# Optimization experiments

Measured on AMD Instinct MI355X. Metric: run time of the kernel, lower is better.

Reference implementation:

```python
import jax, jax.numpy as jnp
import numpy as np

# ---- static config (mirrors GaussianLSS __init__) ----
ORF_H, ORF_W = 256, 704
FC, FH, FW = 128, 32, 88
D_ST, D_END, D_STEP = 4.0, 45.0, 1.0
OUT_C = 128
ERROR_TOL = 1.0
OPACITY_THR = 0.05
XB = (-50.0, 50.0, 1.0)
YB = (-50.0, 50.0, 1.0)
BEV_H = int(round((YB[1] - YB[0]) / YB[2]))
BEV_W = int(round((XB[1] - XB[0]) / XB[2]))
DS = np.arange(D_ST, D_END, D_STEP, dtype=np.float32)
D = DS.shape[0]  # 41
BN_EPS = 1e-3
CHUNK = 512      # gaussians composited per scan step (16896 = 33*512)
B, NCAM = 1, 6


def make_frustum():
    ds = jnp.broadcast_to(jnp.asarray(DS)[:, None, None], (D, FH, FW))
    xs = jnp.broadcast_to(jnp.linspace(0.0, ORF_W - 1.0, FW)[None, None, :], (D, FH, FW))
    ys = jnp.broadcast_to(jnp.linspace(0.0, ORF_H - 1.0, FH)[None, :, None], (D, FH, FW))
    return jnp.stack([xs, ys, ds], -1)  # [D,FH,FW,3]


def get_geometry(rots, trans, intrins, post_rots, post_trans):
    fr = make_frustum()
    pts = fr[None, None] - post_trans[:, :, None, None, None, :]
    pts = jnp.einsum('bnij,bndhwj->bndhwi', jnp.linalg.inv(post_rots), pts)
    pts = jnp.concatenate([pts[..., :2] * pts[..., 2:3], pts[..., 2:3]], -1)
    comb = jnp.einsum('bnij,bnjk->bnik', rots, jnp.linalg.inv(intrins))
    pts = jnp.einsum('bnij,bndhwj->bndhwi', comb, pts) + trans[:, :, None, None, None, :]
    return pts  # [B,N,D,FH,FW,3] ego-frame frustum points


def conv2d(x, w, b, pad):
    y = jax.lax.conv_general_dilated(x, w, (1, 1), [(pad, pad), (pad, pad)],
                                     dimension_numbers=('NCHW', 'OIHW', 'NCHW'))
    return y + b[None, :, None, None]


def bnorm(x, g, bt, m, v):
    s = (g / jnp.sqrt(v + BN_EPS))[None, :, None, None]
    return (x - m[None, :, None, None]) * s + bt[None, :, None, None]


def splat(means, cov6, colors, ops, valid_in):
    # Differentiable BEV gaussian rasterization (3DGS math, orthographic BEV camera,
    # all depths equal -> compositing in stable gaussian-index order).
    H, W = BEV_H, BEV_W
    sh, sw = H / 2.0, W / 2.0  # h/h_meters with FoV=2 (BEVCamera)
    my = -sh * means[:, 1] + H / 2.0  # pixel row (full_proj_transform row 0)
    mx = -sw * means[:, 0] + W / 2.0  # pixel col (row 1)
    a = sh * sh * cov6[:, 3] + 0.3    # 2D cov = J Sigma_xy J^T, +0.3 low-pass as in 3DGS
    c = sw * sw * cov6[:, 0] + 0.3
    b = sh * sw * cov6[:, 1]
    det = a * c - b * b
    valid = valid_in & (det > 0)
    inv_det = jnp.where(det > 0, 1.0 / det, 0.0)
    cA, cB, cC = c * inv_det, -b * inv_det, a * inv_det
    pi = jnp.repeat(jnp.arange(H, dtype=jnp.float32), W)  # [P] pixel rows
    pj = jnp.tile(jnp.arange(W, dtype=jnp.float32), H)    # [P] pixel cols
    G = means.shape[0]
    nchunk = G // CHUNK
    resh = lambda x: x.reshape((nchunk, CHUNK) + x.shape[1:])
    chunks = (resh(my), resh(mx), resh(cA), resh(cB), resh(cC),
              resh(ops), resh(valid), resh(colors))

    def body(carry, ch):
        logT, acc = carry
        my_c, mx_c, A, Bc, Cc, op_c, val_c, col_c = ch
        dI = pi[None, :] - my_c[:, None]                     # [Gc,P]
        dJ = pj[None, :] - mx_c[:, None]
        q = A[:, None] * dI * dI + 2.0 * Bc[:, None] * dI * dJ + Cc[:, None] * dJ * dJ
        alpha = jnp.minimum(0.99, op_c[:, None] * jnp.exp(-0.5 * q))
        alpha = jnp.where(val_c[:, None] & (q >= 0) & (alpha >= 1.0 / 255.0), alpha, 0.0)
        log1m = jnp.log1p(-alpha)
        cum = jnp.cumsum(log1m, axis=0)
        T = jnp.exp(logT[None, :] + cum - log1m)             # transmittance before each gaussian
        acc = acc + jnp.einsum('gp,gc->pc', alpha * T, col_c)
        return (logT + cum[-1], acc), None

    P = H * W
    init = (jnp.zeros((P,), jnp.float32), jnp.zeros((P, colors.shape[1]), jnp.float32))
    (_, acc), _ = jax.lax.scan(jax.checkpoint(body), init, chunks)
    return acc.reshape(H, W, -1).transpose(2, 0, 1)  # [C,H,W], bg is zeros


def _forward(cam2ego_rot, cam2ego_trans, cam_intrins, post_cam2ego_rot, post_cam2ego_trans,
             img_feats, conv1_w, conv1_b, bn1_g, bn1_b, bn1_m, bn1_v,
             conv2_w, conv2_b, bn2_g, bn2_b, bn2_m, bn2_v, conv3_w, conv3_b):
    geom = get_geometry(cam2ego_rot, cam2ego_trans, cam_intrins, post_cam2ego_rot, post_cam2ego_trans)
    b, n = img_feats.shape[:2]
    x = img_feats.reshape(b * n, FC, FH, FW)
    x = jax.nn.relu(bnorm(conv2d(x, conv1_w, conv1_b, 1), bn1_g, bn1_b, bn1_m, bn1_v))
    x = jax.nn.relu(bnorm(conv2d(x, conv2_w, conv2_b, 1), bn2_g, bn2_b, bn2_m, bn2_v))
    x = conv2d(x, conv3_w, conv3_b, 0)
    depth_prob = jax.nn.softmax(x[:, :D], axis=1).reshape(b, n, D, FH, FW)
    opac = jax.nn.sigmoid(x[:, D:D + 1]).reshape(b, n, FH, FW)
    feats = x[:, D + 1:].reshape(b, n, OUT_C, FH, FW)
    # per-pixel gaussian moments of the depth distribution (compute_gaussian)
    means = jnp.einsum('bndhw,bndhwi->bnhwi', depth_prob, geom)
    delta = means[:, :, None] - geom                                       # [B,N,D,FH,FW,3]
    cov = jnp.einsum('bndhw,bndhwi,bndhwj->bnhwij', depth_prob, delta, delta) * (ERROR_TOL ** 2 / 9.0)
    center = jnp.array([(XB[0] + XB[1]) / 2.0, (YB[0] + YB[1]) / 2.0, 0.0], jnp.float32)
    scale = jnp.array([2.0 / (XB[1] - XB[0]), 2.0 / (YB[1] - YB[0]), 1.0], jnp.float32)
    m_n = (means - center) * scale
    cov_n = cov * (scale[:, None] * scale[None, :])
    cov6 = jnp.stack([cov_n[..., 0, 0], cov_n[..., 0, 1], cov_n[..., 0, 2],
                      cov_n[..., 1, 1], cov_n[..., 1, 2], cov_n[..., 2, 2]], -1)
    g = n * FH * FW
    colors = feats.transpose(0, 1, 3, 4, 2).reshape(b, g, OUT_C)
    m_n = m_n.reshape(b, g, 3)
    cov6 = cov6.reshape(b, g, 6)
    ops = opac.reshape(b, g)
    mask = ops > OPACITY_THR  # opacity filtering == zero contribution, order preserved
    bev = jax.vmap(splat)(m_n, cov6, colors, ops, mask)                    # [B,C,H,W]
    num_gaussians = mask.astype(jnp.float32).sum(-1).mean()
    return bev, num_gaussians


def setup_inputs():
    key = jax.random.key(0)
    ks = jax.random.split(key, 8)
    # camera-to-ego rotations: cam->ego axis permutation composed with per-camera yaw
    yaw = np.linspace(0.0, 2.0 * np.pi, NCAM, endpoint=False).astype(np.float32)
    cz, sz = np.cos(yaw), np.sin(yaw)
    rotz = np.zeros((NCAM, 3, 3), np.float32)
    rotz[:, 0, 0] = cz; rotz[:, 0, 1] = -sz
    rotz[:, 1, 0] = sz; rotz[:, 1, 1] = cz
    rotz[:, 2, 2] = 1.0
    perm = np.array([[0.0, 0.0, 1.0], [-1.0, 0.0, 0.0], [0.0, -1.0, 0.0]], np.float32)
    rots = np.einsum('nij,jk->nik', rotz, perm)
    cam2ego_rot = jnp.asarray(np.broadcast_to(rots, (B, NCAM, 3, 3)).copy())
    cam2ego_trans = jax.random.normal(ks[0], (B, NCAM, 3), jnp.float32)
    K = np.array([[600.0, 0.0, ORF_W / 2.0], [0.0, 600.0, ORF_H / 2.0], [0.0, 0.0, 1.0]], np.float32)
    cam_intrins = jnp.asarray(np.broadcast_to(K, (B, NCAM, 3, 3)).copy())
    post_cam2ego_rot = jnp.broadcast_to(jnp.eye(3, dtype=jnp.float32), (B, NCAM, 3, 3)) + jnp.zeros((B, NCAM, 3, 3), jnp.float32)
    post_cam2ego_trans = jnp.zeros((B, NCAM, 3), jnp.float32)
    img_feats = jax.random.normal(ks[1], (B, NCAM, FC, FH, FW), jnp.float32)
    def conv_init(k, o, i, kh, kw):
        return jax.random.normal(k, (o, i, kh, kw), jnp.float32) * (1.0 / np.sqrt(i * kh * kw))
    return dict(cam2ego_rot=cam2ego_rot, cam2ego_trans=cam2ego_trans, cam_intrins=cam_intrins,
                post_cam2ego_rot=post_cam2ego_rot, post_cam2ego_trans=post_cam2ego_trans,
                img_feats=img_feats,
                conv1_w=conv_init(ks[2], FC, FC, 3, 3), conv1_b=jnp.zeros((FC,), jnp.float32),
                bn1_g=jnp.ones((FC,), jnp.float32), bn1_b=jnp.zeros((FC,), jnp.float32),
                bn1_m=jnp.zeros((FC,), jnp.float32), bn1_v=jnp.ones((FC,), jnp.float32),
                conv2_w=conv_init(ks[3], FC, FC, 3, 3), conv2_b=jnp.zeros((FC,), jnp.float32),
                bn2_g=jnp.ones((FC,), jnp.float32), bn2_b=jnp.zeros((FC,), jnp.float32),
                bn2_m=jnp.zeros((FC,), jnp.float32), bn2_v=jnp.ones((FC,), jnp.float32),
                conv3_w=conv_init(ks[4], OUT_C + D + 1, FC, 1, 1),
                conv3_b=jax.random.normal(ks[5], (OUT_C + D + 1,), jnp.float32) * 0.1)


def reference(cam2ego_rot, cam2ego_trans, cam_intrins, post_cam2ego_rot, post_cam2ego_trans,
              img_feats, conv1_w, conv1_b, bn1_g, bn1_b, bn1_m, bn1_v,
              conv2_w, conv2_b, bn2_g, bn2_b, bn2_m, bn2_v, conv3_w, conv3_b):
    return _forward(cam2ego_rot, cam2ego_trans, cam_intrins, post_cam2ego_rot, post_cam2ego_trans,
                    img_feats, conv1_w, conv1_b, bn1_g, bn1_b, bn1_m, bn1_v,
                    conv2_w, conv2_b, bn2_g, bn2_b, bn2_m, bn2_v, conv3_w, conv3_b)
```

## Files before the change

### kernel.cpp

```cpp
#include <hip/hip_runtime.h>

#define NCAM 6
#define FC   128
#define FH_  32
#define FW_  88
#define NPIX (FH_*FW_)
#define PH   34
#define PW   92
#define PPIX (PH*PW)
#define ND   41
#define X3D  42
#define OUTC 128
#define GTOT (NCAM*NPIX)
#define BEVH 100
#define BEVW 100
#define NPXB (BEVH*BEVW)
#define NTILE 25
#define NWORD 264
#define NMASKW (NTILE*NTILE*NWORD)
#define WCAP  70000
#define CSIZE 64
#define CBLK  2048

#define SZA     (NCAM*FC*PPIX)
#define WS_CAM  0
#define WS_A    256
#define WS_RB   (WS_A  + SZA)
#define WS_X3   (WS_RB + SZA)
#define WS_GS   (WS_X3 + NCAM*X3D*NPIX)
#define WS_WL   (WS_GS + GTOT*8)
#define WS_BASE (WS_WL + WCAP)

typedef __attribute__((ext_vector_type(8))) short bf16x8;
typedef __attribute__((ext_vector_type(4))) float f32x4;

__device__ inline unsigned short f2bf(float f) {
    unsigned u = __float_as_uint(f);
    u += 0x7fffu + ((u >> 16) & 1u);
    return (unsigned short)(u >> 16);
}

__device__ inline void inv3x3(const float* m, float* o) {
    float a=m[0],b=m[1],c=m[2],d=m[3],e=m[4],f=m[5],g=m[6],h=m[7],i=m[8];
    float A=e*i-f*h, B=c*h-b*i, C=b*f-c*e;
    float Dd=f*g-d*i, E=a*i-c*g, F=c*d-a*f;
    float Gg=d*h-e*g, H=b*g-a*h, I=a*e-b*d;
    float r = 1.0f/(a*A + b*Dd + c*Gg);
    o[0]=A*r; o[1]=B*r; o[2]=C*r; o[3]=Dd*r; o[4]=E*r; o[5]=F*r;
    o[6]=Gg*r; o[7]=H*r; o[8]=I*r;
}

__global__ __launch_bounds__(256) void pad_input_kernel(const float* __restrict__ src,
        float* __restrict__ dst, float* __restrict__ rb,
        float* __restrict__ outp, unsigned long long* __restrict__ masks) {
    int idx = blockIdx.x*256 + threadIdx.x;
    if (idx < NMASKW) masks[idx] = 0ull;
    if (idx <= NPXB*OUTC) outp[idx] = 0.0f;
    if (idx >= NCAM*FC*PPIX) return;
    int plane = idx / PPIX, pp = idx - plane*PPIX;
    int y = pp / PW, x = pp - y*PW;
    bool interior = (y >= 1 && y <= FH_ && x >= 1 && x <= FW_);
    float v = 0.0f;
    if (interior)
        v = src[(size_t)plane*NPIX + (y-1)*FW_ + (x-1)];
    dst[idx] = v;
    if (!interior) rb[idx] = 0.0f;
}

__global__ __launch_bounds__(128) void conv3x3_pf_kernel(
        const float* __restrict__ in, float* __restrict__ out, const float* __restrict__ w,
        const float* __restrict__ cb, const float* __restrict__ bg, const float* __restrict__ bb,
        const float* __restrict__ bm, const float* __restrict__ bv) {
    const int n   = blockIdx.x;
    const int co0 = blockIdx.y * 4;
    const int qid = blockIdx.z * 128 + threadIdx.x;
    if (qid >= 704) return;
    const int y = qid / 22, x0 = (qid - y*22) * 4;
    float scale[4], shift[4];
    #pragma unroll
    for (int c=0;c<4;c++) {
        float s = bg[co0+c] * rsqrtf(bv[co0+c] + 1e-3f);
        scale[c] = s;
        shift[c] = (cb[co0+c] - bm[co0+c]) * s + bb[co0+c];
    }
    float acc[4][4] = {};
    const float* ip = in + (size_t)n*FC*PPIX + y*PW + x0;
    const float* wb = w + (size_t)co0*FC*9;
    float4 p4[3]; float2 p2[3];
    #pragma unroll
    for (int r=0;r<3;r++) {
        p4[r] = *(const float4*)(ip + r*PW);
        p2[r] = *(const float2*)(ip + r*PW + 4);
    }
    for (int ci=0; ci<FC; ++ci) {
        float v[3][6];
        #pragma unroll
        for (int r=0;r<3;r++) {
            v[r][0]=p4[r].x; v[r][1]=p4[r].y; v[r][2]=p4[r].z; v[r][3]=p4[r].w;
            v[r][4]=p2[r].x; v[r][5]=p2[r].y;
        }
        if (ci + 1 < FC) {
            const float* ipn = ip + PPIX;
            #pragma unroll
            for (int r=0;r<3;r++) {
                p4[r] = *(const float4*)(ipn + r*PW);
                p2[r] = *(const float2*)(ipn + r*PW + 4);
            }
        }
        #pragma unroll
        for (int c=0;c<4;c++) {
            const float* wr = wb + (size_t)c*FC*9 + ci*9;
            float w00=wr[0],w01=wr[1],w02=wr[2],w10=wr[3],w11=wr[4],
                  w12=wr[5],w20=wr[6],w21=wr[7],w22=wr[8];
            #pragma unroll
            for (int p=0;p<4;p++) {
                float a = acc[c][p];
                a = fmaf(w00, v[0][p], a); a = fmaf(w01, v[0][p+1], a); a = fmaf(w02, v[0][p+2], a);
                a = fmaf(w10, v[1][p], a); a = fmaf(w11, v[1][p+1], a); a = fmaf(w12, v[1][p+2], a);
                a = fmaf(w20, v[2][p], a); a = fmaf(w21, v[2][p+1], a); a = fmaf(w22, v[2][p+2], a);
                acc[c][p] = a;
            }
        }
        ip += PPIX;
    }
    const int po = (y+1)*PW + (x0+1);
    #pragma unroll
    for (int c=0;c<4;c++) {
        float* op = out + ((size_t)n*FC + co0 + c)*PPIX + po;
        #pragma unroll
        for (int p=0;p<4;p++)
            op[p] = fmaxf(fmaf(acc[c][p], scale[c], shift[c]), 0.0f);
    }
}

__global__ __launch_bounds__(256) void conv1x1_kernel(const float* __restrict__ in,
        float* __restrict__ x3d, unsigned short* __restrict__ colors16,
        const float* __restrict__ w, const float* __restrict__ b) {
    const int n   = blockIdx.x;
    const int px  = blockIdx.y * 256 + threadIdx.x;
    const int y   = px / FW_, x = px - y*FW_;
    const int pp  = (y+1)*PW + (x+1);
    const float* ip = in + (size_t)n*FC*PPIX + pp;
    if (blockIdx.z < 6) {
        const int co0 = blockIdx.z * 7;
        const float* wr[7];
        float acc[7];
        #pragma unroll
        for (int k=0;k<7;k++) {
            int co = co0 + k;
            wr[k]  = w + (size_t)co*FC;
            acc[k] = b[co];
        }
        #pragma unroll 4
        for (int ci=0; ci<FC; ++ci) {
            float v = ip[(size_t)ci*PPIX];
            #pragma unroll
            for (int k=0;k<7;k++) acc[k] = fmaf(wr[k][ci], v, acc[k]);
        }
        #pragma unroll
        for (int k=0;k<7;k++)
            x3d[((size_t)n*X3D + co0 + k)*NPIX + px] = acc[k];
    } else {
        const int c0  = (blockIdx.z - 6) * 8;
        const int co0 = X3D + c0;
        const float* wr[8];
        float acc[8];
        #pragma unroll
        for (int k=0;k<8;k++) {
            int co = co0 + k;
            wr[k]  = w + (size_t)co*FC;
            acc[k] = b[co];
        }
        #pragma unroll 4
        for (int ci=0; ci<FC; ++ci) {
            float v = ip[(size_t)ci*PPIX];
            #pragma unroll
            for (int k=0;k<8;k++) acc[k] = fmaf(wr[k][ci], v, acc[k]);
        }
        unsigned short h[8];
        #pragma unroll
        for (int k=0;k<8;k++) h[k] = f2bf(acc[k]);
        uint4 pk;
        pk.x = (unsigned)h[0] | ((unsigned)h[1] << 16);
        pk.y = (unsigned)h[2] | ((unsigned)h[3] << 16);
        pk.z = (unsigned)h[4] | ((unsigned)h[5] << 16);
        pk.w = (unsigned)h[6] | ((unsigned)h[7] << 16);
        *(uint4*)(colors16 + (((size_t)(n*NPIX + px)) << 7) + c0) = pk;
    }
}

__global__ __launch_bounds__(256) void moments_kernel(const float* __restrict__ x3,
        const float* __restrict__ rot, const float* __restrict__ tr,
        const float* __restrict__ intr, const float* __restrict__ prot,
        const float* __restrict__ ptr_, float* __restrict__ gauss,
        float* __restrict__ ng) {
    __shared__ float cc[24];
    const int n = blockIdx.x / 11;
    if (threadIdx.x == 0) {
        float M1[9], Ki[9];
        inv3x3(prot + n*9, M1);
        inv3x3(intr + n*9, Ki);
        const float* R = rot + n*9;
        #pragma unroll
        for (int i=0;i<9;i++) cc[i] = M1[i];
        #pragma unroll
        for (int i=0;i<3;i++) cc[9+i] = ptr_[n*3+i];
        #pragma unroll
        for (int i=0;i<3;i++)
            #pragma unroll
            for (int j=0;j<3;j++)
                cc[12+i*3+j] = R[i*3+0]*Ki[0+j] + R[i*3+1]*Ki[3+j] + R[i*3+2]*Ki[6+j];
        #pragma unroll
        for (int i=0;i<3;i++) cc[21+i] = tr[n*3+i];
    }
    __syncthreads();
    const int gi = blockIdx.x*256 + threadIdx.x;
    const int p  = gi - n*NPIX;
    const int h  = p / FW_, xp = p - h*FW_;
    float u = xp * (703.0f/87.0f);
    float v = h  * (255.0f/31.0f);
    float fx = u - cc[9], fy = v - cc[10], fz = -cc[11];
    float p0x = cc[0]*fx + cc[1]*fy + cc[2]*fz;
    float p0y = cc[3]*fx + cc[4]*fy + cc[5]*fz;
    float p0z = cc[6]*fx + cc[7]*fy + cc[8]*fz;
    const float* lg = x3 + (size_t)n*X3D*NPIX + p;

    float lgv[ND];
    #pragma unroll
    for (int d=0; d<ND; ++d) lgv[d] = lg[(size_t)d*NPIX];

    float mxl = -1e30f;
    #pragma unroll
    for (int d=0; d<ND; ++d) mxl = fmaxf(mxl, lgv[d]);

    float s=0.f, sgx=0.f, sgy=0.f;
    #pragma unroll
    for (int d=0; d<ND; ++d) {
        float e  = __expf(lgv[d] - mxl);
        lgv[d] = e;
        float dz = 4.0f + (float)d;
        float pz = p0z + dz*cc[8];
        float px = (p0x + dz*cc[2]) * pz;
        float py = (p0y + dz*cc[5]) * pz;
        float gx = cc[12]*px + cc[13]*py + cc[14]*pz + cc[21];
        float gy = cc[15]*px + cc[16]*py + cc[17]*pz + cc[22];
        s += e; sgx += e*gx; sgy += e*gy;
    }
    float inv_s = 1.0f/s;
    float mex = sgx*inv_s, mey = sgy*inv_s;
    float cxx=0.f, cxy=0.f, cyy=0.f;
    #pragma unroll
    for (int d=0; d<ND; ++d) {
        float e  = lgv[d];
        float dz = 4.0f + (float)d;
        float pz = p0z + dz*cc[8];
        float px = (p0x + dz*cc[2]) * pz;
        float py = (p0y + dz*cc[5]) * pz;
        float gx = cc[12]*px + cc[13]*py + cc[14]*pz + cc[21];
        float gy = cc[15]*px + cc[16]*py + cc[17]*pz + cc[22];
        float dxv = gx - mex, dyv = gy - mey;
        cxx += e*dxv*dxv; cxy += e*dxv*dyv; cyy += e*dyv*dyv;
    }
    const float k9 = inv_s * (1.0f/9.0f);
    cxx *= k9; cxy *= k9; cyy *= k9;

    float lo = lg[(size_t)ND*NPIX];
    float op = 1.0f/(1.0f + __expf(-lo));
    bool mask = op > 0.05f;

    const float SC = 0.02f, SH = 50.0f, SW = 50.0f;
    float my = -SH*(mey*SC) + 50.0f;
    float mx = -SW*(mex*SC) + 50.0f;
    float a  = SH*SH*(cyy*SC*SC) + 0.3f;
    float b  = SH*SW*(cxy*SC*SC);
    float c  = SW*SW*(cxx*SC*SC) + 0.3f;
    float det = a*c - b*b;
    bool valid = mask && (det > 0.0f);
    float A, B2, C, qm, ri, rj;
    if (valid) {
        float idet = 1.0f/det;
        A = c*idet; B2 = -2.0f*b*idet; C = a*idet;
        qm = 2.0f*__logf(255.0f*op);
        ri = sqrtf(qm*a); rj = sqrtf(qm*c);
    } else { A=B2=C=0.f; qm=-1.0f; ri=-1e30f; rj=-1e30f; }
    float* gp = gauss + (size_t)gi*8;
    gp[0]=my; gp[1]=mx; gp[2]=A; gp[3]=B2; gp[4]=C; gp[5]=qm; gp[6]=ri; gp[7]=rj;

    unsigned long long bal = __ballot(mask);
    if ((threadIdx.x & 63) == 0) atomicAdd(ng, (float)__popcll(bal));
}

__global__ __launch_bounds__(256) void scatter_masks_kernel(const float* __restrict__ gauss,
        unsigned long long* __restrict__ masks) {
    const int idx = blockIdx.x*256 + threadIdx.x;
    const int g = idx >> 2, q = idx & 3;
    const float4 g0 = *(const float4*)(gauss + ((size_t)g << 3));
    const float4 g1 = *(const float4*)(gauss + ((size_t)g << 3) + 4);
    if (g1.y < 0.0f) return;
    const float my = g0.x, mx = g0.y, A = g0.z, B = 0.5f*g0.w, C = g1.x, qm = g1.y, ri = g1.z;
    const float invC = 1.0f / C;
    const float k2 = C*A - B*B;
    int ti0 = max(0, (int)floorf((my - ri) * 0.25f));
    int ti1 = min(NTILE-1, (int)floorf((my + ri) * 0.25f));
    int len = ti1 - ti0 + 1;
    int ta = ti0 + (len*q) / 4;
    int tb = ti0 + (len*(q+1)) / 4;
    const int wi = g >> 6;
    const unsigned long long bit = 1ull << (g & 63);
    for (int ti = ta; ti < tb; ++ti) {
        float jmn = 1e30f, jmx = -1e30f;
        #pragma unroll
        for (int r = 0; r < 4; ++r) {
            int i = 4*ti + r;
            if (i < 0 || i > 99) continue;
            float di = (float)i - my;
            float disc = C*qm - k2*di*di;
            if (disc < 0.0f) continue;
            float sd = sqrtf(disc);
            float jc = -B*di;
            jmn = fminf(jmn, (jc - sd)*invC + mx);
            jmx = fmaxf(jmx, (jc + sd)*invC + mx);
        }
        if (jmx < jmn) continue;
        int jl = max(0, (int)ceilf(jmn));
        int jh = min(99, (int)floorf(jmx));
        if (jl > jh) continue;
        for (int tj = (jl >> 2); tj <= (jh >> 2); ++tj)
            atomicOr(&masks[(size_t)(ti*NTILE + tj)*NWORD + wi], bit);
    }
}

__global__ __launch_bounds__(256) void cnt_kernel(const unsigned long long* __restrict__ masks,
                                                  int* __restrict__ cnt) {
    __shared__ int sc;
    const int tile = blockIdx.x, t = threadIdx.x;
    if (t == 0) sc = 0;
    __syncthreads();
    if (t < NWORD) atomicAdd(&sc, __popcll(masks[(size_t)tile*NWORD + t]));
    __syncthreads();
    if (t == 0) cnt[tile] = sc;
}

__global__ __launch_bounds__(640) void scan_kernel(const int* __restrict__ cnt,
        int* __restrict__ off, int* __restrict__ choff, int* __restrict__ nwork) {
    __shared__ int wsum[16], wsum2[16];
    const int t = threadIdx.x;
    const int lane = t & 63, wv = t >> 6;
    int c  = (t < NTILE*NTILE) ? cnt[t] : 0;
    int ch = (c + CSIZE-1) >> 6;
    int v = c, v2 = ch;
    #pragma unroll
    for (int o = 1; o < 64; o <<= 1) {
        int u  = __shfl_up(v,  (unsigned)o, 64);
        int u2 = __shfl_up(v2, (unsigned)o, 64);
        if (lane >= o) { v += u; v2 += u2; }
    }
    if (lane == 63) { wsum[wv] = v; wsum2[wv] = v2; }
    __syncthreads();
    int pre = 0, pre2 = 0;
    for (int w2 = 0; w2 < wv; ++w2) { pre += wsum[w2]; pre2 += wsum2[w2]; }
    int inc = v + pre, inc2 = v2 + pre2;
    if (t < NTILE*NTILE) { off[t] = inc - c; choff[t] = inc2 - ch; }
    if (t == NTILE*NTILE - 1) {
        off[NTILE*NTILE] = inc;
        choff[NTILE*NTILE] = inc2;
        nwork[0] = (inc2 > WCAP) ? WCAP : inc2;
    }
}

__global__ __launch_bounds__(256) void fill_kernel(const unsigned long long* __restrict__ masks,
        const int* __restrict__ cnt, const int* __restrict__ off, const int* __restrict__ choff,
        unsigned short* __restrict__ list, int* __restrict__ wl) {
    __shared__ unsigned long long sw[NWORD];
    __shared__ int wpre[NWORD];
    const int tile = blockIdx.x, t = threadIdx.x;
    if (t < NWORD) sw[t] = masks[(size_t)tile*NWORD + t];
    __syncthreads();
    if (t == 0) {
        int run = 0;
        for (int w2 = 0; w2 < NWORD; ++w2) { wpre[w2] = run; run += __popcll(sw[w2]); }
    }
    __syncthreads();
    if (t < NWORD) {
        unsigned long long m = sw[t];
        int pos = off[tile] + wpre[t], base = t << 6;
        while (m) { int b = __builtin_ctzll(m); m &= m - 1; list[pos++] = (unsigned short)(base + b); }
    }
    int nch = (cnt[tile] + CSIZE-1)/CSIZE;
    int c0 = choff[tile];
    if (t < nch && c0 + t < WCAP) wl[c0 + t] = (tile << 9) | t;
}

__device__ inline float eval_alpha(const float4 g0, const float4 g1, float fi, float fj) {
    float dI = fi - g0.x, dJ = fj - g0.y;
    float q = dI*(g0.z*dI + g0.w*dJ) + g1.x*dJ*dJ;
    if (q < 0.0f || q > g1.y) return 0.0f;
    return fminf(0.99f, 0.003921568627f * __expf(0.5f*(g1.y - q)));
}

__global__ __launch_bounds__(256) void chunk_sums_kernel(const float* __restrict__ gauss,
        const unsigned short* __restrict__ list, const int* __restrict__ cnt,
        const int* __restrict__ off, const int* __restrict__ wl, const int* __restrict__ nwork,
        float* __restrict__ base) {
    const int nw = nwork[0];
    const int lane = threadIdx.x & 63;
    const int wid  = (blockIdx.x * 256 + threadIdx.x) >> 6;
    const int nwv  = (gridDim.x * 256) >> 6;
    const int px = lane & 15, kg = lane >> 4;
    for (int e = wid; e < nw; e += nwv) {
        int v = wl[e], tile = v >> 9, c = v & 511;
        int hbase = off[tile] + (c << 6);
        int nh = min(CSIZE, cnt[tile] - (c << 6));
        const int i0 = (tile / NTILE) * 4, j0 = (tile % NTILE) * 4;
        const float fi = (float)(i0 + (px >> 2)), fj = (float)(j0 + (px & 3));
        float s = 1.0f;
        for (int k = kg; k < nh; k += 4) {
            int g = list[hbase + k];
            float4 g0 = *(const float4*)(gauss + ((size_t)g << 3));
            float4 g1 = *(const float4*)(gauss + ((size_t)g << 3) + 4);
            float a = eval_alpha(g0, g1, fi, fj);
            s *= (1.0f - a);
        }
        s *= __shfl_xor(s, 16, 64);
        s *= __shfl_xor(s, 32, 64);
        if (lane < 16) base[(size_t)e*16 + lane] = s;
    }
}

__global__ __launch_bounds__(256) void chunk_prefix_kernel(const int* __restrict__ choff,
                                                           float* __restrict__ base) {
    __shared__ float part[16][17];
    const int tile = blockIdx.x, t = threadIdx.x;
    const int c0 = choff[tile], nch = choff[tile+1] - c0;
    if (nch == 0) return;
    const int px = t & 15, cg = t >> 4;
    const int L16 = (nch + 15) >> 4;
    const int a0 = cg*L16, a1 = min(nch, a0 + L16);
    float s = 1.0f;
    for (int c = a0; c < a1; ++c) s *= base[(size_t)(c0 + c)*16 + px];
    part[cg][px] = s;
    __syncthreads();
    if (t < 16) {
        float run = 1.0f;
        #pragma unroll
        for (int k = 0; k < 16; ++k) { float tmp = part[k][t]; part[k][t] = run; run *= tmp; }
    }
    __syncthreads();
    float run = part[cg][px];
    for (int c = a0; c < a1; ++c) {
        size_t idx = (size_t)(c0 + c)*16 + px;
        float tmp = base[idx];
        base[idx] = run;
        run *= tmp;
    }
}

__global__ __launch_bounds__(256) void composite_kernel(const float* __restrict__ gauss,
        const unsigned short* __restrict__ colors16, const unsigned short* __restrict__ list,
        const int* __restrict__ cnt, const int* __restrict__ off, const int* __restrict__ wl,
        const int* __restrict__ nwork, const float* __restrict__ base, float* __restrict__ out) {
    const int nw = nwork[0];
    const int t = threadIdx.x;
    const int lane = t & 63;
    const int e_px = t >> 4, e_kg = t & 15;
    const int wv_id = t >> 6;
    const int m16 = lane & 15;
    const int kb  = lane >> 4;
    const int chA = (wv_id << 5) + m16;
    const int chB = chA + 16;
    const int f_pxq = t >> 5;
    const int f_r0  = f_pxq >> 2, f_j = f_pxq & 3;
    const int cs4r  = t & 31;
    __shared__ unsigned short slist[2][CSIZE];
    __shared__ unsigned short s_w16[8][16][8];
    __shared__ float fred[128*17];
    const int per = (nw + CBLK - 1) / CBLK;
    int e0 = blockIdx.x * per;
    if (e0 >= nw) return;
    int e1 = min(nw, e0 + per);

    f32x4 accA = {0.f,0.f,0.f,0.f};
    f32x4 accB = {0.f,0.f,0.f,0.f};
    int cur_tile = wl[e0] >> 9;
    int cur_i0 = (cur_tile / NTILE) * 4, cur_j0 = (cur_tile % NTILE) * 4;

    int buf = 0;
    {
        int v = wl[e0], tl = v >> 9, c = v & 511;
        int nh0 = min(CSIZE, cnt[tl] - (c << 6));
        if (t < CSIZE) slist[0][t] = (t < nh0) ? list[off[tl] + (c << 6) + t] : 0;
    }

    for (int e = e0; e < e1; ++e) {
        int v = wl[e], tile = v >> 9, c = v & 511;
        const bool tflush = (tile != cur_tile);
        const int fi0 = cur_i0, fj0 = cur_j0;
        if (tflush) {
            const int cs4A = (wv_id << 3) + (m16 >> 2);
            const int compA = m16 & 3;
            #pragma unroll
            for (int r = 0; r < 4; ++r) {
                fred[((kb << 5) + cs4A)*17 + (r << 2) + compA]     = accA[r];
                fred[((kb << 5) + cs4A + 4)*17 + (r << 2) + compA] = accB[r];
            }
            accA = (f32x4){0.f,0.f,0.f,0.f};
            accB = (f32x4){0.f,0.f,0.f,0.f};
            cur_tile = tile;
            cur_i0 = (tile / NTILE) * 4; cur_j0 = (tile % NTILE) * 4;
        }
        const int nh = min(CSIZE, cnt[tile] - (c << 6));
        __syncthreads();
        if (tflush) {
            const float* f0 = &fred[(f_r0*32 + cs4r)*17 + (f_j<<2)];
            const float* f1 = &fred[((f_r0+2)*32 + cs4r)*17 + (f_j<<2)];
            const int pix0 = (fi0 + f_r0) * BEVW + fj0 + f_j;
            const int pix1 = pix0 + 2 * BEVW;
            float* op = out + (size_t)(cs4r << 2) * NPXB;
            atomicAdd(op + 0*NPXB + pix0, f0[0]); atomicAdd(op + 1*NPXB + pix0, f0[1]);
            atomicAdd(op + 2*NPXB + pix0, f0[2]); atomicAdd(op + 3*NPXB + pix0, f0[3]);
            atomicAdd(op + 0*NPXB + pix1, f1[0]); atomicAdd(op + 1*NPXB + pix1, f1[1]);
            atomicAdd(op + 2*NPXB + pix1, f1[2]); atomicAdd(op + 3*NPXB + pix1, f1[3]);
        }
        if (e + 1 < e1) {
            int v2 = wl[e+1], tl2 = v2 >> 9, c2 = v2 & 511;
            int nh2 = min(CSIZE, cnt[tl2] - (c2 << 6));
            if (t < CSIZE) slist[buf^1][t] = (t < nh2) ? list[off[tl2] + (c2 << 6) + t] : 0;
        }
        {
            const float fi = (float)(cur_i0 + (e_px >> 2)), fj = (float)(cur_j0 + (e_px & 3));
            const int k0 = e_kg << 2;
            float a4[4]; float p = 1.0f;
            #pragma unroll
            for (int i = 0; i < 4; ++i) {
                int k = k0 + i;
                float a = 0.0f;
                if (k < nh) {
                    int g = slist[buf][k];
                    float4 g0 = *(const float4*)(gauss + ((size_t)g << 3));
                    float4 g1 = *(const float4*)(gauss + ((size_t)g << 3) + 4);
                    a = eval_alpha(g0, g1, fi, fj);
                }
                a4[i] = a;
                p *= (1.0f - a);
            }
            float s = p;
            #pragma unroll
            for (int o = 1; o < 16; o <<= 1) {
                float u = __shfl_up(s, (unsigned)o, 64);
                if ((lane & 15) >= o) s *= u;
            }
            float ex = __shfl_up(s, 1u, 64);
            float T = base[(size_t)e*16 + e_px] * (((lane & 15) == 0) ? 1.0f : ex);
            unsigned short* swp = &s_w16[e_kg >> 1][e_px][(e_kg & 1) << 2];
            #pragma unroll
            for (int i = 0; i < 4; ++i) {
                float wvv = a4[i] * T; T -= wvv;
                swp[i] = f2bf(wvv);
            }
        }
        __syncthreads();
        {
            #pragma unroll
            for (int s = 0; s < 2; ++s) {
                bf16x8 afrag = *(const bf16x8*)&s_w16[(s << 2) + kb][m16][0];
                const int kbase = (s << 5) + (kb << 3);
                bf16x8 bA, bB;
                #pragma unroll
                for (int j = 0; j < 8; ++j) {
                    int g = slist[buf][kbase + j];
                    const unsigned short* cp = colors16 + ((size_t)g << 7);
                    bA[j] = (short)cp[chA];
                    bB[j] = (short)cp[chB];
                }
                accA = __builtin_amdgcn_mfma_f32_16x16x32_bf16(afrag, bA, accA, 0, 0, 0);
                accB = __builtin_amdgcn_mfma_f32_16x16x32_bf16(afrag, bB, accB, 0, 0, 0);
            }
        }
        buf ^= 1;
    }
    {
        const int cs4A = (wv_id << 3) + (m16 >> 2);
        const int compA = m16 & 3;
        #pragma unroll
        for (int r = 0; r < 4; ++r) {
            fred[((kb << 5) + cs4A)*17 + (r << 2) + compA]     = accA[r];
            fred[((kb << 5) + cs4A + 4)*17 + (r << 2) + compA] = accB[r];
        }
    }
    __syncthreads();
    {
        const float* f0 = &fred[(f_r0*32 + cs4r)*17 + (f_j<<2)];
        const float* f1 = &fred[((f_r0+2)*32 + cs4r)*17 + (f_j<<2)];
        const int pix0 = (cur_i0 + f_r0) * BEVW + cur_j0 + f_j;
        const int pix1 = pix0 + 2 * BEVW;
        float* op = out + (size_t)(cs4r << 2) * NPXB;
        atomicAdd(op + 0*NPXB + pix0, f0[0]); atomicAdd(op + 1*NPXB + pix0, f0[1]);
        atomicAdd(op + 2*NPXB + pix0, f0[2]); atomicAdd(op + 3*NPXB + pix0, f0[3]);
        atomicAdd(op + 0*NPXB + pix1, f1[0]); atomicAdd(op + 1*NPXB + pix1, f1[1]);
        atomicAdd(op + 2*NPXB + pix1, f1[2]); atomicAdd(op + 3*NPXB + pix1, f1[3]);
    }
}

extern "C" void kernel_launch(void* const* d_in, const int* in_sizes, int n_in,
                              void* d_out, int out_size, void* d_ws, size_t ws_size,
                              hipStream_t stream) {
    const float* rot  = (const float*)d_in[0];
    const float* tr   = (const float*)d_in[1];
    const float* intr = (const float*)d_in[2];
    const float* prot = (const float*)d_in[3];
    const float* ptr_ = (const float*)d_in[4];
    const float* img  = (const float*)d_in[5];
    const float* c1w  = (const float*)d_in[6];  const float* c1b = (const float*)d_in[7];
    const float* b1g  = (const float*)d_in[8];  const float* b1b = (const float*)d_in[9];
    const float* b1m  = (const float*)d_in[10]; const float* b1v = (const float*)d_in[11];
    const float* c2w  = (const float*)d_in[12]; const float* c2b = (const float*)d_in[13];
    const float* b2g  = (const float*)d_in[14]; const float* b2b = (const float*)d_in[15];
    const float* b2m  = (const float*)d_in[16]; const float* b2v = (const float*)d_in[17];
    const float* c3w  = (const float*)d_in[18]; const float* c3b = (const float*)d_in[19];
    float* out = (float*)d_out;
    float* ws  = (float*)d_ws;
    float* RA  = ws + WS_A;
    float* RB  = ws + WS_RB;
    float* X3B = ws + WS_X3;
    float* GS  = ws + WS_GS;
    int*   WL  = (int*)(ws + WS_WL);
    float* BASE = ws + WS_BASE;
    unsigned long long* MASKS = (unsigned long long*)BASE;
    int* AUXI = (int*)(ws + WS_X3 + 330000);
    int* CNT = AUXI;
    int* OFF = AUXI + 640;
    int* CHOFF = AUXI + 1280;
    int* NWORK = AUXI + 1920;
    unsigned short* LIST = (unsigned short*)RA;
    unsigned short* COL16 = (unsigned short*)RB;
    float* ngp = out + (size_t)NPXB*OUTC;

    pad_input_kernel<<<(NCAM*FC*PPIX + 255)/256, 256, 0, stream>>>(img, RA, RB, out, MASKS);
    conv3x3_pf_kernel<<<dim3(NCAM,32,6), 128, 0, stream>>>(RA, RB, c1w, c1b, b1g, b1b, b1m, b1v);
    conv3x3_pf_kernel<<<dim3(NCAM,32,6), 128, 0, stream>>>(RB, RA, c2w, c2b, b2g, b2b, b2m, b2v);
    conv1x1_kernel<<<dim3(NCAM,11,22), 256, 0, stream>>>(RA, X3B, COL16, c3w, c3b);
    moments_kernel<<<GTOT/256, 256, 0, stream>>>(X3B, rot, tr, intr, prot, ptr_, GS, ngp);
    scatter_masks_kernel<<<GTOT*4/256, 256, 0, stream>>>(GS, MASKS);
    cnt_kernel<<<NTILE*NTILE, 256, 0, stream>>>(MASKS, CNT);
    scan_kernel<<<1, 640, 0, stream>>>(CNT, OFF, CHOFF, NWORK);
    fill_kernel<<<NTILE*NTILE, 256, 0, stream>>>(MASKS, CNT, OFF, CHOFF, LIST, WL);
    chunk_sums_kernel<<<8192, 256, 0, stream>>>(GS, LIST, CNT, OFF, WL, NWORK, BASE);
    chunk_prefix_kernel<<<NTILE*NTILE, 256, 0, stream>>>(CHOFF, BASE);
    composite_kernel<<<CBLK, 256, 0, stream>>>(GS, COL16, LIST, CNT, OFF, WL, NWORK, BASE, out);
}
```

Before: 456.6 us.

## Process two same-tile chunks per iteration in composite kernel

The composite loop now handles two consecutive work items of the same tile in one iteration. Their alpha evaluations, prefix-product scans and MFMA accumulations are interleaved, which halves the number of block-wide barriers per chunk and exposes more independent memory loads. Gaussian index lists are prefetched up to two items ahead into a 4-slot ring buffer, and the weight staging array is padded to 17 rows to reduce LDS bank conflicts. In exchange, register pressure rises from the duplicated fragments and the control flow gets more complex.

```diff
diff --git a/kernel.cpp b/kernel.cpp
--- a/kernel.cpp
+++ b/kernel.cpp
@@ -471,8 +471,8 @@
     const int f_pxq = t >> 5;
     const int f_r0  = f_pxq >> 2, f_j = f_pxq & 3;
     const int cs4r  = t & 31;
-    __shared__ unsigned short slist[2][CSIZE];
-    __shared__ unsigned short s_w16[8][16][8];
+    __shared__ unsigned short slist[4][CSIZE];
+    __shared__ unsigned short s_w16[2][8][17][8];
     __shared__ float fred[128*17];
     const int per = (nw + CBLK - 1) / CBLK;
     int e0 = blockIdx.x * per;
@@ -484,15 +484,21 @@
     int cur_tile = wl[e0] >> 9;
     int cur_i0 = (cur_tile / NTILE) * 4, cur_j0 = (cur_tile % NTILE) * 4;
 
-    int buf = 0;
-    {
-        int v = wl[e0], tl = v >> 9, c = v & 511;
-        int nh0 = min(CSIZE, cnt[tl] - (c << 6));
-        if (t < CSIZE) slist[0][t] = (t < nh0) ? list[off[tl] + (c << 6) + t] : 0;
-    }
-
-    for (int e = e0; e < e1; ++e) {
+    int L = e0;
+    for (; L < e1 && L < e0 + 2; ++L) {
+        int v = wl[L], tl = v >> 9, c = v & 511;
+        int nhl = min(CSIZE, cnt[tl] - (c << 6));
+        if (t < CSIZE) slist[L & 3][t] = (t < nhl) ? list[off[tl] + (c << 6) + t] : 0;
+    }
+
+    int e = e0;
+    while (e < e1) {
         int v = wl[e], tile = v >> 9, c = v & 511;
+        bool pair = false; int c2 = 0;
+        if (e + 1 < e1) {
+            int v2 = wl[e+1];
+            if ((v2 >> 9) == tile) { pair = true; c2 = v2 & 511; }
+        }
         const bool tflush = (tile != cur_tile);
         const int fi0 = cur_i0, fj0 = cur_j0;
         if (tflush) {
@@ -508,7 +514,8 @@
             cur_tile = tile;
             cur_i0 = (tile / NTILE) * 4; cur_j0 = (tile % NTILE) * 4;
         }
-        const int nh = min(CSIZE, cnt[tile] - (c << 6));
+        const int nh  = min(CSIZE, cnt[tile] - (c << 6));
+        const int nh2 = pair ? min(CSIZE, cnt[tile] - (c2 << 6)) : 0;
         __syncthreads();
         if (tflush) {
             const float* f0 = &fred[(f_r0*32 + cs4r)*17 + (f_j<<2)];
@@ -521,62 +528,109 @@
             atomicAdd(op + 0*NPXB + pix1, f1[0]); atomicAdd(op + 1*NPXB + pix1, f1[1]);
             atomicAdd(op + 2*NPXB + pix1, f1[2]); atomicAdd(op + 3*NPXB + pix1, f1[3]);
         }
-        if (e + 1 < e1) {
-            int v2 = wl[e+1], tl2 = v2 >> 9, c2 = v2 & 511;
-            int nh2 = min(CSIZE, cnt[tl2] - (c2 << 6));
-            if (t < CSIZE) slist[buf^1][t] = (t < nh2) ? list[off[tl2] + (c2 << 6) + t] : 0;
+        {
+            const int target = min(e1, e + (pair ? 2 : 1) + 2);
+            for (; L < target; ++L) {
+                int vv = wl[L], tl = vv >> 9, cc = vv & 511;
+                int nhl = min(CSIZE, cnt[tl] - (cc << 6));
+                if (t < CSIZE) slist[L & 3][t] = (t < nhl) ? list[off[tl] + (cc << 6) + t] : 0;
+            }
         }
         {
             const float fi = (float)(cur_i0 + (e_px >> 2)), fj = (float)(cur_j0 + (e_px & 3));
             const int k0 = e_kg << 2;
-            float a4[4]; float p = 1.0f;
+            float a4a[4], a4b[4];
+            float p1 = 1.0f, p2 = 1.0f;
             #pragma unroll
             for (int i = 0; i < 4; ++i) {
                 int k = k0 + i;
-                float a = 0.0f;
+                float aa = 0.0f, ab = 0.0f;
                 if (k < nh) {
-                    int g = slist[buf][k];
+                    int g = slist[e & 3][k];
                     float4 g0 = *(const float4*)(gauss + ((size_t)g << 3));
                     float4 g1 = *(const float4*)(gauss + ((size_t)g << 3) + 4);
-                    a = eval_alpha(g0, g1, fi, fj);
+                    aa = eval_alpha(g0, g1, fi, fj);
                 }
-                a4[i] = a;
-                p *= (1.0f - a);
-            }
-            float s = p;
+                if (k < nh2) {
+                    int g = slist[(e+1) & 3][k];
+                    float4 g0 = *(const float4*)(gauss + ((size_t)g << 3));
+                    float4 g1 = *(const float4*)(gauss + ((size_t)g << 3) + 4);
+                    ab = eval_alpha(g0, g1, fi, fj);
+                }
+                a4a[i] = aa; a4b[i] = ab;
+                p1 *= (1.0f - aa);
+                p2 *= (1.0f - ab);
+            }
+            float sa = p1, sb = p2;
             #pragma unroll
             for (int o = 1; o < 16; o <<= 1) {
-                float u = __shfl_up(s, (unsigned)o, 64);
-                if ((lane & 15) >= o) s *= u;
-            }
-            float ex = __shfl_up(s, 1u, 64);
-            float T = base[(size_t)e*16 + e_px] * (((lane & 15) == 0) ? 1.0f : ex);
-            unsigned short* swp = &s_w16[e_kg >> 1][e_px][(e_kg & 1) << 2];
+                float ua = __shfl_up(sa, (unsigned)o, 64);
+                float ub = __shfl_up(sb, (unsigned)o, 64);
+                if ((lane & 15) >= o) { sa *= ua; sb *= ub; }
+            }
+            float exa = __shfl_up(sa, 1u, 64);
+            float exb = __shfl_up(sb, 1u, 64);
+            const bool l0 = ((lane & 15) == 0);
+            float Ta = base[(size_t)e*16 + e_px] * (l0 ? 1.0f : exa);
+            unsigned short* swpa = &s_w16[0][e_kg >> 1][e_px][(e_kg & 1) << 2];
             #pragma unroll
             for (int i = 0; i < 4; ++i) {
-                float wvv = a4[i] * T; T -= wvv;
-                swp[i] = f2bf(wvv);
+                float wv_ = a4a[i] * Ta; Ta -= wv_;
+                swpa[i] = f2bf(wv_);
+            }
+            if (pair) {
+                float Tb = base[(size_t)(e+1)*16 + e_px] * (l0 ? 1.0f : exb);
+                unsigned short* swpb = &s_w16[1][e_kg >> 1][e_px][(e_kg & 1) << 2];
+                #pragma unroll
+                for (int i = 0; i < 4; ++i) {
+                    float wv_ = a4b[i] * Tb; Tb -= wv_;
+                    swpb[i] = f2bf(wv_);
+                }
             }
         }
         __syncthreads();
         {
-            #pragma unroll
-            for (int s = 0; s < 2; ++s) {
-                bf16x8 afrag = *(const bf16x8*)&s_w16[(s << 2) + kb][m16][0];
-                const int kbase = (s << 5) + (kb << 3);
-                bf16x8 bA, bB;
+            bf16x8 af0 = *(const bf16x8*)&s_w16[0][kb][m16][0];
+            bf16x8 af1 = *(const bf16x8*)&s_w16[0][4 + kb][m16][0];
+            bf16x8 bA0, bB0, bA1, bB1;
+            #pragma unroll
+            for (int j = 0; j < 8; ++j) {
+                int g0i = slist[e & 3][(kb << 3) + j];
+                int g1i = slist[e & 3][32 + (kb << 3) + j];
+                const unsigned short* cp0 = colors16 + ((size_t)g0i << 7);
+                const unsigned short* cp1 = colors16 + ((size_t)g1i << 7);
+                bA0[j] = (short)cp0[chA]; bB0[j] = (short)cp0[chB];
+                bA1[j] = (short)cp1[chA]; bB1[j] = (short)cp1[chB];
+            }
+            if (pair) {
+                bf16x8 cf0 = *(const bf16x8*)&s_w16[1][kb][m16][0];
+                bf16x8 cf1 = *(const bf16x8*)&s_w16[1][4 + kb][m16][0];
+                bf16x8 dA0, dB0, dA1, dB1;
                 #pragma unroll
                 for (int j = 0; j < 8; ++j) {
-                    int g = slist[buf][kbase + j];
-                    const unsigned short* cp = colors16 + ((size_t)g << 7);
-                    bA[j] = (short)cp[chA];
-                    bB[j] = (short)cp[chB];
+                    int g0i = slist[(e+1) & 3][(kb << 3) + j];
+                    int g1i = slist[(e+1) & 3][32 + (kb << 3) + j];
+                    const unsigned short* cp0 = colors16 + ((size_t)g0i << 7);
+                    const unsigned short* cp1 = colors16 + ((size_t)g1i << 7);
+                    dA0[j] = (short)cp0[chA]; dB0[j] = (short)cp0[chB];
+                    dA1[j] = (short)cp1[chA]; dB1[j] = (short)cp1[chB];
                 }
-                accA = __builtin_amdgcn_mfma_f32_16x16x32_bf16(afrag, bA, accA, 0, 0, 0);
-                accB = __builtin_amdgcn_mfma_f32_16x16x32_bf16(afrag, bB, accB, 0, 0, 0);
-            }
-        }
-        buf ^= 1;
+                accA = __builtin_amdgcn_mfma_f32_16x16x32_bf16(af0, bA0, accA, 0, 0, 0);
+                accB = __builtin_amdgcn_mfma_f32_16x16x32_bf16(af0, bB0, accB, 0, 0, 0);
+                accA = __builtin_amdgcn_mfma_f32_16x16x32_bf16(af1, bA1, accA, 0, 0, 0);
+                accB = __builtin_amdgcn_mfma_f32_16x16x32_bf16(af1, bB1, accB, 0, 0, 0);
+                accA = __builtin_amdgcn_mfma_f32_16x16x32_bf16(cf0, dA0, accA, 0, 0, 0);
+                accB = __builtin_amdgcn_mfma_f32_16x16x32_bf16(cf0, dB0, accB, 0, 0, 0);
+                accA = __builtin_amdgcn_mfma_f32_16x16x32_bf16(cf1, dA1, accA, 0, 0, 0);
+                accB = __builtin_amdgcn_mfma_f32_16x16x32_bf16(cf1, dB1, accB, 0, 0, 0);
+            } else {
+                accA = __builtin_amdgcn_mfma_f32_16x16x32_bf16(af0, bA0, accA, 0, 0, 0);
+                accB = __builtin_amdgcn_mfma_f32_16x16x32_bf16(af0, bB0, accB, 0, 0, 0);
+                accA = __builtin_amdgcn_mfma_f32_16x16x32_bf16(af1, bA1, accA, 0, 0, 0);
+                accB = __builtin_amdgcn_mfma_f32_16x16x32_bf16(af1, bB1, accB, 0, 0, 0);
+            }
+        }
+        e += pair ? 2 : 1;
     }
     {
         const int cs4A = (wv_id << 3) + (m16 >> 2);
```

New measurement: 451.5 us. Within noise of the previous version (-1.1%).
